# Kernel tuning notes

Hardware: AMD Instinct MI355X
Metric: run time of the kernel (lower is better)

The kernel has to match this reference:

```python
import jax, jax.numpy as jnp
import numpy as np
import math

B, N, F0, HID, OUT, K = 8, 2048, 128, 64, 16, 10


def setup_inputs() -> dict:
    key = jax.random.key(0)
    ks = jax.random.split(key, 6)
    X = jax.random.normal(ks[0], (B, N, F0), dtype=jnp.float32)
    # Row-stochastic dense 'rescaled Laplacian': spectrum inside unit disk,
    # so K-th order Bernstein polynomial stays numerically stable.
    A = jax.random.uniform(ks[1], (N, N), dtype=jnp.float32)
    L = A / jnp.sum(A, axis=1, keepdims=True)
    W1 = jax.random.normal(ks[2], (F0, HID), dtype=jnp.float32) / np.float32(np.sqrt(F0))
    b1 = jnp.zeros((HID,), dtype=jnp.float32)
    W2 = jax.random.normal(ks[3], (HID, OUT), dtype=jnp.float32) / np.float32(np.sqrt(HID))
    b2 = jnp.zeros((OUT,), dtype=jnp.float32)
    theta = 0.02 * jax.random.normal(ks[4], (K + 1,), dtype=jnp.float32)
    return {"X": X, "L": L, "W1": W1, "b1": b1, "W2": W2, "b2": b2,
            "theta": theta, "dp": 0}


def _bern_filter(Hf, L, theta, binom):
    # g(L) Hf = sum_i theta_i C(K,i) L^i (I-L)^{K-i} Hf
    # Computed by applying L / (I-L) directly to the (B,N,F) features
    # (mathematically identical to forming the NxN basis matrices).
    Lap = lambda Y: jnp.einsum('vw,bwf->bvf', L, Y)
    ys = [Hf]                       # ys[k] = (I-L)^k Hf
    for _ in range(K):
        ys.append(ys[-1] - Lap(ys[-1]))
    a = theta * binom               # (K+1,)
    # Horner in L: r = a_K Hf; r <- L r + a_i (I-L)^{K-i} Hf
    r = a[K] * Hf
    for i in range(K - 1, -1, -1):
        r = Lap(r) + a[i] * ys[K - i]
    return r


def reference(X, L, W1, b1, W2, b2, theta, dp):
    binom = jnp.asarray([math.comb(K, i) for i in range(K + 1)], dtype=X.dtype)
    # dropout with p=dp=0 is identity
    Hf = jax.nn.relu(X @ W1 + b1)          # (B, N, HID)
    Hf = _bern_filter(Hf, L, theta, binom) # (B, N, HID)
    Hg = jnp.mean(Hf, axis=1)              # (B, HID)
    logits = Hg @ W2 + b2                  # (B, OUT)
    return logits
```

## Files before the change

kernel.cpp:

```cpp
#include <hip/hip_runtime.h>

#define NN     2048
#define F0D    128
#define HIDD   64
#define OUTD   16
#define KDEG   10
#define NCHAIN 128
#define COLS   16

typedef unsigned int u32;

#define CTAG(j) (0xC0DE0000u + (u32)(j))
#define HTAG    0xBEEF0001u

static __device__ __forceinline__ u32 ld_flag(const u32* p) {
    return __hip_atomic_load(p, __ATOMIC_RELAXED, __HIP_MEMORY_SCOPE_AGENT);
}
static __device__ __forceinline__ void st_flag(u32* p, u32 v) {
    __hip_atomic_store(p, v, __ATOMIC_RELAXED, __HIP_MEMORY_SCOPE_AGENT);
}
static __device__ __forceinline__ void st_data(float* p, float v) {
    __hip_atomic_store(p, v, __ATOMIC_RELAXED, __HIP_MEMORY_SCOPE_AGENT);
}

__global__ __launch_bounds__(256, 1) void k_fused(
    const float* __restrict__ X, const float* __restrict__ L,
    const float* __restrict__ W1, const float* __restrict__ b1,
    const float* __restrict__ W2, const float* __restrict__ b2,
    const float* __restrict__ theta, float* __restrict__ out,
    float* __restrict__ ws)
{
    float* PB  = ws;
    u32*   FLH = (u32*)(ws + 49152);
    float* Hg  = ws + 51200;

    __shared__ union {
        struct { float Lt[NN * COLS]; float redf[4][16]; float cbv[16]; int rdy[16]; } mv;
        struct { float W1t[64][132]; float redm[16][65]; float wv[64]; } hd;
    } sm;

    const int g = blockIdx.x;
    const int t = threadIdx.x;

    if (g < NCHAIN) {
        const int u0 = g * COLS;

        if (t <= KDEG) {
            const float C10[11] = {1,10,45,120,210,252,210,120,45,10,1};
            float acc = 0.f;
            for (int i = 0; i <= t; ++i) {
                int n = KDEG - i, r = t - i;
                long long cm = 1;
                for (int s = 1; s <= r; ++s) cm = cm * (n - r + s) / s;
                float term = theta[i] * C10[i] * (float)cm;
                if ((t - i) & 1) term = -term;
                acc += term;
            }
            sm.mv.cbv[t] = acc;
        }
        if (t < 16) sm.mv.rdy[t] = 0;

        const float4* L4  = (const float4*)L;
        float4*       Lt4 = (float4*)sm.mv.Lt;
        const int qc = t & 3, r0 = t >> 2;
        {
            float4 acc = make_float4(0.f, 0.f, 0.f, 0.f);
            #pragma unroll 8
            for (int i = 0; i < 32; ++i) {
                int v = r0 + 64 * i;
                float4 lv = L4[(size_t)v * (NN / 4) + (u0 >> 2) + qc];
                Lt4[v * 4 + qc] = lv;
                acc.x += lv.x; acc.y += lv.y; acc.z += lv.z; acc.w += lv.w;
            }
            #pragma unroll
            for (int m = 4; m <= 32; m <<= 1) {
                acc.x += __shfl_xor(acc.x, m); acc.y += __shfl_xor(acc.y, m);
                acc.z += __shfl_xor(acc.z, m); acc.w += __shfl_xor(acc.w, m);
            }
            int lane = t & 63, wid = t >> 6;
            if (lane < 4) *(float4*)&sm.mv.redf[wid][lane * 4] = acc;
        }
        __syncthreads();

        float val = 0.f, wacc = 0.f;
        if (t < COLS) {
            float s = sm.mv.redf[0][t] + sm.mv.redf[1][t]
                    + sm.mv.redf[2][t] + sm.mv.redf[3][t];
            val = s; wacc = sm.mv.cbv[0];
            st_data(&PB[u0 + t], s);
        }
        if (t < 64) {
            asm volatile("s_waitcnt vmcnt(0)" ::: "memory");
            if (t == 0) st_flag(((u32*)(ws + 28672)) + g * 16, CTAG(1));
        }

        for (int j = 2; j <= KDEG; ++j) {
            if (t < 64) {
                const u32* fb = (const u32*)(ws + 28672 + (size_t)(j - 2) * 2048);
                const u32 tag = CTAG(j - 1);
                const u32* f0 = fb + t * 16;
                const u32* f1 = fb + (t + 64) * 16;
                while (!__all(ld_flag(f0) == tag && ld_flag(f1) == tag))
                    __builtin_amdgcn_s_sleep(1);
                asm volatile("" ::: "memory");
                if (t == 0) ((volatile int*)sm.mv.rdy)[j] = 1;
            } else {
                volatile int* vr = (volatile int*)sm.mv.rdy;
                while (vr[j] == 0) __builtin_amdgcn_s_sleep(1);
                asm volatile("" ::: "memory");
            }

            const float* psrc = PB + (size_t)(j - 2) * 2048;
            float4 a2 = make_float4(0.f, 0.f, 0.f, 0.f);
            #pragma unroll 8
            for (int k = 0; k < 32; ++k) {
                int v = r0 + 64 * k;
                float xv = psrc[v];
                float4 lv = Lt4[v * 4 + qc];
                a2.x += lv.x * xv; a2.y += lv.y * xv;
                a2.z += lv.z * xv; a2.w += lv.w * xv;
            }
            #pragma unroll
            for (int m = 4; m <= 32; m <<= 1) {
                a2.x += __shfl_xor(a2.x, m); a2.y += __shfl_xor(a2.y, m);
                a2.z += __shfl_xor(a2.z, m); a2.w += __shfl_xor(a2.w, m);
            }
            {
                int lane = t & 63, wid = t >> 6;
                if (lane < 4) *(float4*)&sm.mv.redf[wid][lane * 4] = a2;
            }
            __syncthreads();

            if (t < COLS) {
                float s = sm.mv.redf[0][t] + sm.mv.redf[1][t]
                        + sm.mv.redf[2][t] + sm.mv.redf[3][t];
                wacc += sm.mv.cbv[j - 1] * val;
                val = s;
                float outv = (j < KDEG) ? s : (wacc + sm.mv.cbv[KDEG] * s);
                st_data(&PB[(size_t)(j - 1) * 2048 + u0 + t], outv);
            }
            if (t < 64) {
                asm volatile("s_waitcnt vmcnt(0)" ::: "memory");
                if (t == 0)
                    st_flag(((u32*)(ws + 28672 + (size_t)(j - 1) * 2048)) + g * 16,
                            CTAG(j));
            }
        }

        if (g == 0) {
            if (t < 64) {
                for (;;) {
                    int ok = (ld_flag(FLH + t * 16) == HTAG)
                           & (ld_flag(FLH + (t + 64) * 16) == HTAG);
                    if (__all(ok)) break;
                    __builtin_amdgcn_s_sleep(2);
                }
                asm volatile("" ::: "memory");
            }
            __syncthreads();
            if (t < 128) {
                int o = t & 15, bb = t >> 4;
                float a3 = b2[o];
                #pragma unroll
                for (int h = 0; h < HIDD; ++h)
                    a3 += Hg[bb * 64 + h] * W2[h * 16 + o];
                out[bb * 16 + o] = a3;
            }
        }
        return;
    }

    const int u = g - NCHAIN;
    const int vchunk = u & 31, bA = u >> 5, bB = bA + 4;

    if (t == 0) {
        const u32* fp = ((const u32*)(ws + 28672)) + u * 16;
        while (ld_flag(fp) != CTAG(1)) __builtin_amdgcn_s_sleep(2);
    }
    __syncthreads();

    for (int i = t; i < F0D * HIDD; i += 256) {
        int f = i >> 6, h = i & 63;
        sm.hd.W1t[h][f] = W1[i];
    }
    __syncthreads();

    const int hg = t & 15, vg = t >> 4;
    const int vbase = vchunk * 64 + vg * 4;
    const float* XA = X + ((size_t)bA * NN + vbase) * F0D;
    const float* XB = X + ((size_t)bB * NN + vbase) * F0D;
    float accA[4][4] = {}, accB[4][4] = {};
    for (int f = 0; f < F0D; f += 4) {
        float4 xa[4], xb[4];
        #pragma unroll
        for (int i = 0; i < 4; ++i) {
            xa[i] = *(const float4*)(XA + (size_t)i * F0D + f);
            xb[i] = *(const float4*)(XB + (size_t)i * F0D + f);
        }
        #pragma unroll
        for (int jj = 0; jj < 4; ++jj) {
            float4 wr = *(const float4*)(&sm.hd.W1t[hg + 16 * jj][f]);
            #pragma unroll
            for (int i = 0; i < 4; ++i) {
                accA[i][jj] += xa[i].x * wr.x + xa[i].y * wr.y
                             + xa[i].z * wr.z + xa[i].w * wr.w;
                accB[i][jj] += xb[i].x * wr.x + xb[i].y * wr.y
                             + xb[i].z * wr.z + xb[i].w * wr.w;
            }
        }
    }

    if (t < 4) {
        const u32* fp = ((u32*)(ws + 28672 + (size_t)(KDEG - 1) * 2048))
                      + (vchunk * 4 + t) * 16;
        while (ld_flag(fp) != CTAG(KDEG)) __builtin_amdgcn_s_sleep(2);
        asm volatile("" ::: "memory");
    }
    __syncthreads();
    if (t < 16)
        ((float4*)sm.hd.wv)[t] =
            ((const float4*)(PB + (size_t)(KDEG - 1) * 2048 + vchunk * 64))[t];
    __syncthreads();

    const float inv = 1.0f / (float)NN;
    float hsA[4] = {0.f,0.f,0.f,0.f}, hsB[4] = {0.f,0.f,0.f,0.f};
    #pragma unroll
    for (int i = 0; i < 4; ++i) {
        float we = sm.hd.wv[vg * 4 + i];
        #pragma unroll
        for (int jj = 0; jj < 4; ++jj) {
            float rA = accA[i][jj] + b1[hg + 16 * jj];
            float rB = accB[i][jj] + b1[hg + 16 * jj];
            rA = rA > 0.f ? rA : 0.f;
            rB = rB > 0.f ? rB : 0.f;
            hsA[jj] += rA * we;
            hsB[jj] += rB * we;
        }
    }
    #pragma unroll
    for (int jj = 0; jj < 4; ++jj) sm.hd.redm[vg][hg + 16 * jj] = hsA[jj];
    __syncthreads();
    if (t < 64) {
        float s = 0.f;
        #pragma unroll
        for (int i = 0; i < 16; ++i) s += sm.hd.redm[i][t];
        atomicAdd(&Hg[bA * 64 + t], s * inv);
    }
    __syncthreads();
    #pragma unroll
    for (int jj = 0; jj < 4; ++jj) sm.hd.redm[vg][hg + 16 * jj] = hsB[jj];
    __syncthreads();
    if (t < 64) {
        float s = 0.f;
        #pragma unroll
        for (int i = 0; i < 16; ++i) s += sm.hd.redm[i][t];
        atomicAdd(&Hg[bB * 64 + t], s * inv);
        asm volatile("s_waitcnt vmcnt(0)" ::: "memory");
        if (t == 0) st_flag(FLH + u * 16, HTAG);
    }
}

extern "C" void kernel_launch(void* const* d_in, const int* in_sizes, int n_in,
                              void* d_out, int out_size, void* d_ws, size_t ws_size,
                              hipStream_t stream) {
    const float* X     = (const float*)d_in[0];
    const float* L     = (const float*)d_in[1];
    const float* W1    = (const float*)d_in[2];
    const float* b1    = (const float*)d_in[3];
    const float* W2    = (const float*)d_in[4];
    const float* b2    = (const float*)d_in[5];
    const float* theta = (const float*)d_in[6];
    float* outp = (float*)d_out;
    float* wsp  = (float*)d_ws;

    hipMemsetAsync((char*)d_ws + 49152 * sizeof(float), 0, 10240, stream);

    hipLaunchKernelGGL(k_fused, dim3(256), dim3(256), 0, stream,
                       X, L, W1, b1, W2, b2, theta, outp, wsp);
}
```

Before: 124.9 us.

## Pack sync flags contiguously and batch-load chain vector before matvec

Flags that were padded 64 bytes apart are now packed densely (one u32 per block). Polling waves therefore read them with coalesced loads, and the workspace memset shrinks. The matvec loop now issues all 32 vector loads up front into registers, which lets them overlap in flight rather than being interleaved with the FMAs. Packing the flags can create false sharing on cache lines, and the register array raises VGPR pressure.

```diff
diff --git a/kernel.cpp b/kernel.cpp
--- a/kernel.cpp
+++ b/kernel.cpp
@@ -31,8 +31,9 @@
     float* __restrict__ ws)
 {
     float* PB  = ws;
+    u32*   FLC = (u32*)(ws + 28672);
     u32*   FLH = (u32*)(ws + 49152);
-    float* Hg  = ws + 51200;
+    float* Hg  = ws + 49280;
 
     __shared__ union {
         struct { float Lt[NN * COLS]; float redf[4][16]; float cbv[16]; int rdy[16]; } mv;
@@ -91,16 +92,14 @@
         }
         if (t < 64) {
             asm volatile("s_waitcnt vmcnt(0)" ::: "memory");
-            if (t == 0) st_flag(((u32*)(ws + 28672)) + g * 16, CTAG(1));
+            if (t == 0) st_flag(FLC + g, CTAG(1));
         }
 
         for (int j = 2; j <= KDEG; ++j) {
             if (t < 64) {
-                const u32* fb = (const u32*)(ws + 28672 + (size_t)(j - 2) * 2048);
+                const u32* fb = FLC + (size_t)(j - 2) * 128;
                 const u32 tag = CTAG(j - 1);
-                const u32* f0 = fb + t * 16;
-                const u32* f1 = fb + (t + 64) * 16;
-                while (!__all(ld_flag(f0) == tag && ld_flag(f1) == tag))
+                while (!__all(ld_flag(fb + t) == tag && ld_flag(fb + t + 64) == tag))
                     __builtin_amdgcn_s_sleep(1);
                 asm volatile("" ::: "memory");
                 if (t == 0) ((volatile int*)sm.mv.rdy)[j] = 1;
@@ -111,14 +110,16 @@
             }
 
             const float* psrc = PB + (size_t)(j - 2) * 2048;
+            float xv[32];
+            #pragma unroll
+            for (int k = 0; k < 32; ++k) xv[k] = psrc[r0 + 64 * k];
+
             float4 a2 = make_float4(0.f, 0.f, 0.f, 0.f);
-            #pragma unroll 8
+            #pragma unroll
             for (int k = 0; k < 32; ++k) {
-                int v = r0 + 64 * k;
-                float xv = psrc[v];
-                float4 lv = Lt4[v * 4 + qc];
-                a2.x += lv.x * xv; a2.y += lv.y * xv;
-                a2.z += lv.z * xv; a2.w += lv.w * xv;
+                float4 lv = Lt4[(r0 + 64 * k) * 4 + qc];
+                a2.x += lv.x * xv[k]; a2.y += lv.y * xv[k];
+                a2.z += lv.z * xv[k]; a2.w += lv.w * xv[k];
             }
             #pragma unroll
             for (int m = 4; m <= 32; m <<= 1) {
@@ -141,17 +142,15 @@
             }
             if (t < 64) {
                 asm volatile("s_waitcnt vmcnt(0)" ::: "memory");
-                if (t == 0)
-                    st_flag(((u32*)(ws + 28672 + (size_t)(j - 1) * 2048)) + g * 16,
-                            CTAG(j));
+                if (t == 0) st_flag(FLC + (size_t)(j - 1) * 128 + g, CTAG(j));
             }
         }
 
         if (g == 0) {
             if (t < 64) {
                 for (;;) {
-                    int ok = (ld_flag(FLH + t * 16) == HTAG)
-                           & (ld_flag(FLH + (t + 64) * 16) == HTAG);
+                    int ok = (ld_flag(FLH + t) == HTAG)
+                           & (ld_flag(FLH + t + 64) == HTAG);
                     if (__all(ok)) break;
                     __builtin_amdgcn_s_sleep(2);
                 }
@@ -174,8 +173,7 @@
     const int vchunk = u & 31, bA = u >> 5, bB = bA + 4;
 
     if (t == 0) {
-        const u32* fp = ((const u32*)(ws + 28672)) + u * 16;
-        while (ld_flag(fp) != CTAG(1)) __builtin_amdgcn_s_sleep(2);
+        while (ld_flag(FLC + u) != CTAG(1)) __builtin_amdgcn_s_sleep(2);
     }
     __syncthreads();
 
@@ -211,8 +209,7 @@
     }
 
     if (t < 4) {
-        const u32* fp = ((u32*)(ws + 28672 + (size_t)(KDEG - 1) * 2048))
-                      + (vchunk * 4 + t) * 16;
+        const u32* fp = FLC + (size_t)(KDEG - 1) * 128 + vchunk * 4 + t;
         while (ld_flag(fp) != CTAG(KDEG)) __builtin_amdgcn_s_sleep(2);
         asm volatile("" ::: "memory");
     }
@@ -256,7 +253,7 @@
         for (int i = 0; i < 16; ++i) s += sm.hd.redm[i][t];
         atomicAdd(&Hg[bB * 64 + t], s * inv);
         asm volatile("s_waitcnt vmcnt(0)" ::: "memory");
-        if (t == 0) st_flag(FLH + u * 16, HTAG);
+        if (t == 0) st_flag(FLH + u, HTAG);
     }
 }
 
@@ -273,7 +270,7 @@
     float* outp = (float*)d_out;
     float* wsp  = (float*)d_ws;
 
-    hipMemsetAsync((char*)d_ws + 49152 * sizeof(float), 0, 10240, stream);
+    hipMemsetAsync((char*)d_ws + 49152 * sizeof(float), 0, 2560, stream);
 
     hipLaunchKernelGGL(k_fused, dim3(256), dim3(256), 0, stream,
                        X, L, W1, b1, W2, b2, theta, outp, wsp);
```

Result: slower. 132.3 us (+5.9%).
